# Kernel tuning notes

Measured on AMD Instinct MI355X. Metric: run time of the kernel, lower is better.

The kernel has to match this reference:

```python
import jax, jax.numpy as jnp
import numpy as np

N, F, E, T = 50000, 128, 800000, 8


def setup_inputs() -> dict:
    key = jax.random.key(0)
    ks = jax.random.split(key, 10)
    s = 1.0 / np.sqrt(F)
    return {
        "x": jax.random.normal(ks[0], (N, F), jnp.float32),
        "edge_index": jax.random.randint(ks[1], (2, E), 0, N, jnp.int64),
        "edge_weight": jax.random.uniform(ks[2], (E,), jnp.float32),
        "W0": jax.random.normal(ks[3], (F, F), jnp.float32) * s,
        "Wih": jax.random.normal(ks[4], (3 * F, F), jnp.float32) * s,
        "Whh": jax.random.normal(ks[5], (3 * F, F), jnp.float32) * s,
        "bih": jax.random.normal(ks[6], (3 * F,), jnp.float32) * s,
        "bhh": jax.random.normal(ks[7], (3 * F,), jnp.float32) * s,
        "Wlin": jax.random.normal(ks[8], (T, F), jnp.float32) * s,
        "blin": jax.random.normal(ks[9], (T,), jnp.float32) * s,
    }


def _evolve_weight(W0, Wih, Whh, bih, bhh):
    # One GRU step with input = hidden = W0 (rows of weight matrix as batch).
    gi = W0 @ Wih.T + bih  # [F, 3F]
    gh = W0 @ Whh.T + bhh
    ir, iz, inn = jnp.split(gi, 3, axis=1)
    hr, hz, hn = jnp.split(gh, 3, axis=1)
    r = jax.nn.sigmoid(ir + hr)
    z = jax.nn.sigmoid(iz + hz)
    n = jnp.tanh(inn + r * hn)
    return (1.0 - z) * n + z * W0  # [F, F]


def reference(x, edge_index, edge_weight, W0, Wih, Whh, bih, bhh, Wlin, blin):
    n_nodes = x.shape[0]
    W = _evolve_weight(W0, Wih, Whh, bih, bhh)
    # gcn_norm with added self-loops (fill value 1.0), symmetric normalization
    loop = jnp.arange(n_nodes, dtype=edge_index.dtype)
    row = jnp.concatenate([edge_index[0], loop])
    col = jnp.concatenate([edge_index[1], loop])
    ew = jnp.concatenate([edge_weight, jnp.ones((n_nodes,), edge_weight.dtype)])
    deg = jax.ops.segment_sum(ew, col, num_segments=n_nodes)
    dinv = jnp.where(deg > 0, jax.lax.rsqrt(jnp.where(deg > 0, deg, 1.0)), 0.0)
    norm = dinv[row] * ew * dinv[col]  # [E+N]
    xw = x @ W  # [N, F]
    h = jax.ops.segment_sum(norm[:, None] * xw[row], col, num_segments=n_nodes)
    h = jax.nn.relu(h)
    return h @ Wlin.T + blin  # [N, n_target]
```

## Files before the change

### kernel.cpp

```cpp
#include <hip/hip_runtime.h>
#include <math.h>

#define F 128
#define FIX_SCALE 16777216.0f
#define FIX_INV   (1.0f / 16777216.0f)
#define CNT_SHIFT 40
#define DEG_MASK  ((1ULL << 40) - 1)

using bf16x8 = __attribute__((ext_vector_type(8))) short;
using f32x4  = __attribute__((ext_vector_type(4))) float;

__device__ inline int read_idx(const int* ei, long long elem, int i64) {
    return i64 ? (int)((const long long*)ei)[elem] : ei[elem];
}
__device__ inline unsigned int f2bf_rn(float f) {
    unsigned int b = __float_as_uint(f);
    return (b + 0x7FFFu + ((b >> 16) & 1u)) >> 16;
}
__device__ inline float bflo(unsigned int u) { return __uint_as_float(u << 16); }
__device__ inline float bfhi(unsigned int u) { return __uint_as_float(u & 0xFFFF0000u); }

__global__ void k_init(unsigned long long* packed, int* flag, const int* ei, int N) {
    int i = blockIdx.x * blockDim.x + threadIdx.x;
    if (i < N) packed[i] = 0ULL;
    if (i == 0) {
        int i64 = 1;
        for (int j = 0; j < 32; ++j) if (ei[2 * j + 1] != 0) { i64 = 0; break; }
        *flag = i64;
    }
}

__global__ void k_count(const int* ei, const float* ew, unsigned long long* packed,
                        int* pos, const int* flag, int E) {
    int e = blockIdx.x * blockDim.x + threadIdx.x;
    if (e >= E) return;
    int i64 = *flag;
    int c = read_idx(ei, (long long)E + e, i64);
    unsigned long long u = (1ULL << CNT_SHIFT) |
                           (unsigned long long)(ew[e] * FIX_SCALE + 0.5f);
    unsigned long long old = atomicAdd(&packed[c], u);
    pos[e] = (int)(old >> CNT_SHIFT);
}

__global__ void k_bsum(const unsigned long long* __restrict__ packed,
                       int* __restrict__ bsum, int N) {
    __shared__ int s[4];
    int i = blockIdx.x * 256 + threadIdx.x;
    int v = (i < N) ? (int)(packed[i] >> CNT_SHIFT) : 0;
    #pragma unroll
    for (int o = 1; o < 64; o <<= 1) v += __shfl_xor(v, o, 64);
    if ((threadIdx.x & 63) == 0) s[threadIdx.x >> 6] = v;
    __syncthreads();
    if (threadIdx.x == 0) bsum[blockIdx.x] = s[0] + s[1] + s[2] + s[3];
}

__global__ void k_bscan(int* bsum, int nb) {
    __shared__ int sdata[1024];
    int tid = threadIdx.x;
    int run = 0;
    for (int base = 0; base < nb; base += 1024) {
        int i = base + tid;
        int v = (i < nb) ? bsum[i] : 0;
        sdata[tid] = v;
        __syncthreads();
        #pragma unroll
        for (int s = 1; s < 1024; s <<= 1) {
            int add = (tid >= s) ? sdata[tid - s] : 0;
            __syncthreads();
            sdata[tid] += add;
            __syncthreads();
        }
        if (i < nb) bsum[i] = run + sdata[tid] - v;
        run += sdata[1023];
        __syncthreads();
    }
}

__global__ void k_offs(const unsigned long long* __restrict__ packed,
                       const int* __restrict__ bsum,
                       int* __restrict__ off, float* __restrict__ dinv, int N, int E) {
    __shared__ int sdata[256];
    int t = threadIdx.x;
    int i = blockIdx.x * 256 + t;
    unsigned long long p = (i < N) ? packed[i] : 0ULL;
    int v = (int)(p >> CNT_SHIFT);
    sdata[t] = v;
    __syncthreads();
    #pragma unroll
    for (int s = 1; s < 256; s <<= 1) {
        int add = (t >= s) ? sdata[t - s] : 0;
        __syncthreads();
        sdata[t] += add;
        __syncthreads();
    }
    if (i < N) {
        off[i] = bsum[blockIdx.x] + sdata[t] - v;
        float deg = 1.0f + (float)(p & DEG_MASK) * FIX_INV;
        dinv[i] = rsqrtf(deg);
        if (i == N - 1) off[N] = E;
    }
}

__global__ void k_place(const int* ei, const float* ew,
                        const int* __restrict__ off, const int* __restrict__ pos,
                        int2* ep, const int* flag, int E) {
    int e = blockIdx.x * blockDim.x + threadIdx.x;
    if (e >= E) return;
    int i64 = *flag;
    int r = read_idx(ei, e, i64);
    int c = read_idx(ei, (long long)E + e, i64);
    ep[off[c] + pos[e]] = make_int2(r, __float_as_int(ew[e]));
}

__global__ void k_evolve(const float* __restrict__ W0, const float* __restrict__ Wih,
                         const float* __restrict__ Whh, const float* __restrict__ bih,
                         const float* __restrict__ bhh,
                         unsigned short* __restrict__ Wth,
                         unsigned short* __restrict__ Wtl) {
    __shared__ __align__(16) float w0row[F];
    int i = blockIdx.x;
    int j = threadIdx.x;
    w0row[j] = W0[i * F + j];
    __syncthreads();
    float air = 0, aiz = 0, ain = 0, ahr = 0, ahz = 0, ahn = 0;
    const float* ir_p = Wih + (size_t)j * F;
    const float* iz_p = Wih + (size_t)(j + F) * F;
    const float* in_p = Wih + (size_t)(j + 2 * F) * F;
    const float* hr_p = Whh + (size_t)j * F;
    const float* hz_p = Whh + (size_t)(j + F) * F;
    const float* hn_p = Whh + (size_t)(j + 2 * F) * F;
    for (int k = 0; k < F; k += 4) {
        float4 w0 = *(const float4*)&w0row[k];
        float4 a;
        a = *(const float4*)&ir_p[k]; air += w0.x*a.x + w0.y*a.y + w0.z*a.z + w0.w*a.w;
        a = *(const float4*)&iz_p[k]; aiz += w0.x*a.x + w0.y*a.y + w0.z*a.z + w0.w*a.w;
        a = *(const float4*)&in_p[k]; ain += w0.x*a.x + w0.y*a.y + w0.z*a.z + w0.w*a.w;
        a = *(const float4*)&hr_p[k]; ahr += w0.x*a.x + w0.y*a.y + w0.z*a.z + w0.w*a.w;
        a = *(const float4*)&hz_p[k]; ahz += w0.x*a.x + w0.y*a.y + w0.z*a.z + w0.w*a.w;
        a = *(const float4*)&hn_p[k]; ahn += w0.x*a.x + w0.y*a.y + w0.z*a.z + w0.w*a.w;
    }
    air += bih[j];         ahr += bhh[j];
    aiz += bih[j + F];     ahz += bhh[j + F];
    ain += bih[j + 2*F];   ahn += bhh[j + 2*F];
    float r = 1.0f / (1.0f + expf(-(air + ahr)));
    float z = 1.0f / (1.0f + expf(-(aiz + ahz)));
    float n = tanhf(ain + r * ahn);
    float w = (1.0f - z) * n + z * w0row[j];
    unsigned int hb = f2bf_rn(w);
    float whi = __uint_as_float(hb << 16);
    unsigned int lb = f2bf_rn(w - whi);
    Wth[j * F + i] = (unsigned short)hb;
    Wtl[j * F + i] = (unsigned short)lb;
}

__global__ void k_cast(const float2* __restrict__ x2, const float* __restrict__ dinv,
                       unsigned int* __restrict__ xs, int M ) {
    int id = blockIdx.x * 256 + threadIdx.x;
    if (id >= M) return;
    float di = dinv[id >> 6];
    float2 v = x2[id];
    xs[id] = f2bf_rn(di * v.x) | (f2bf_rn(di * v.y) << 16);
}

__global__ __launch_bounds__(256) void k_agg2(const uint4* __restrict__ xs4,
                                              const int* __restrict__ off,
                                              const int2* __restrict__ ep,
                                              const float* __restrict__ dinv,
                                              uint4* __restrict__ hagg4, int N) {
    int wave = threadIdx.x >> 6, lane = threadIdx.x & 63;
    int c = blockIdx.x * 4 + wave;
    if (c >= N) return;
    int g = lane >> 4, sl = lane & 15;
    int start = off[c], end = off[c + 1];
    float a0[8] = {0,0,0,0,0,0,0,0}, a1[8] = {0,0,0,0,0,0,0,0};
    if (g == 0) {
        uint4 v = xs4[(size_t)c * 16 + sl];
        a0[0] = bflo(v.x); a0[1] = bfhi(v.x);
        a0[2] = bflo(v.y); a0[3] = bfhi(v.y);
        a0[4] = bflo(v.z); a0[5] = bfhi(v.z);
        a0[6] = bflo(v.w); a0[7] = bfhi(v.w);
    }
    for (int k = start; k < end; k += 8) {
        int iA = k + g, iB = k + g + 4;
        bool okA = iA < end, okB = iB < end;
        int2 eA, eB;
        if (okA) eA = ep[iA];
        if (okB) eB = ep[iB];
        if (okA) {
            uint4 v = xs4[(size_t)eA.x * 16 + sl];
            float w = __int_as_float(eA.y);
            a0[0] += w * bflo(v.x); a0[1] += w * bfhi(v.x);
            a0[2] += w * bflo(v.y); a0[3] += w * bfhi(v.y);
            a0[4] += w * bflo(v.z); a0[5] += w * bfhi(v.z);
            a0[6] += w * bflo(v.w); a0[7] += w * bfhi(v.w);
        }
        if (okB) {
            uint4 v = xs4[(size_t)eB.x * 16 + sl];
            float w = __int_as_float(eB.y);
            a1[0] += w * bflo(v.x); a1[1] += w * bfhi(v.x);
            a1[2] += w * bflo(v.y); a1[3] += w * bfhi(v.y);
            a1[4] += w * bflo(v.z); a1[5] += w * bfhi(v.z);
            a1[6] += w * bflo(v.w); a1[7] += w * bfhi(v.w);
        }
    }
    #pragma unroll
    for (int f = 0; f < 8; ++f) {
        float v = a0[f] + a1[f];
        v += __shfl_xor(v, 16, 64);
        v += __shfl_xor(v, 32, 64);
        a0[f] = v;
    }
    if (lane < 16) {
        float di = dinv[c];
        uint4 o;
        o.x = f2bf_rn(di * a0[0]) | (f2bf_rn(di * a0[1]) << 16);
        o.y = f2bf_rn(di * a0[2]) | (f2bf_rn(di * a0[3]) << 16);
        o.z = f2bf_rn(di * a0[4]) | (f2bf_rn(di * a0[5]) << 16);
        o.w = f2bf_rn(di * a0[6]) | (f2bf_rn(di * a0[7]) << 16);
        hagg4[(size_t)c * 16 + lane] = o;
    }
}

__global__ __launch_bounds__(256) void k_gemm(const uint4* __restrict__ hagg4,
                                              const unsigned short* __restrict__ Wth,
                                              const unsigned short* __restrict__ Wtl,
                                              const float* __restrict__ Wlin,
                                              const float* __restrict__ blin,
                                              float* __restrict__ out, int N) {
    __shared__ __align__(16) unsigned int At[64 * 68];
    __shared__ __align__(16) float WlinL[8 * F];
    int t = threadIdx.x;
    int row0 = blockIdx.x * 64;
    #pragma unroll
    for (int it = 0; it < 4; ++it) {
        int idx = it * 256 + t;
        int rr = idx >> 4, c4 = idx & 15;
        uint4 v = make_uint4(0u, 0u, 0u, 0u);
        if (row0 + rr < N) v = hagg4[(size_t)(row0 + rr) * 16 + c4];
        *(uint4*)&At[rr * 68 + c4 * 4] = v;
    }
    *(float4*)&WlinL[t * 4] = *(const float4*)&Wlin[t * 4];
    __syncthreads();

    int wave = t >> 6, lane = t & 63;
    int sl = lane & 15, q = lane >> 4;
    const unsigned short* Ash = (const unsigned short*)At;
    int mrow = wave * 16 + sl;

    f32x4 acc[8];
    #pragma unroll
    for (int nt = 0; nt < 8; ++nt) acc[nt] = (f32x4){0.f, 0.f, 0.f, 0.f};
    #pragma unroll
    for (int ko = 0; ko < 4; ++ko) {
        bf16x8 a = *(const bf16x8*)&Ash[mrow * 136 + ko * 32 + q * 8];
        #pragma unroll
        for (int nt = 0; nt < 8; ++nt) {
            int boff = (nt * 16 + sl) * F + ko * 32 + q * 8;
            bf16x8 bh = *(const bf16x8*)&Wth[boff];
            bf16x8 bl = *(const bf16x8*)&Wtl[boff];
            acc[nt] = __builtin_amdgcn_mfma_f32_16x16x32_bf16(a, bh, acc[nt], 0, 0, 0);
            acc[nt] = __builtin_amdgcn_mfma_f32_16x16x32_bf16(a, bl, acc[nt], 0, 0, 0);
        }
    }
    #pragma unroll
    for (int nt = 0; nt < 8; ++nt)
        #pragma unroll
        for (int r = 0; r < 4; ++r) acc[nt][r] = fmaxf(acc[nt][r], 0.f);

    float p[8][4];
    #pragma unroll
    for (int tt = 0; tt < 8; ++tt) {
        float wl[8];
        #pragma unroll
        for (int nt = 0; nt < 8; ++nt) wl[nt] = WlinL[tt * F + nt * 16 + sl];
        #pragma unroll
        for (int r = 0; r < 4; ++r) {
            float s = 0.f;
            #pragma unroll
            for (int nt = 0; nt < 8; ++nt) s += acc[nt][r] * wl[nt];
            p[tt][r] = s;
        }
    }
    #pragma unroll
    for (int tt = 0; tt < 8; ++tt)
        #pragma unroll
        for (int r = 0; r < 4; ++r) {
            float v = p[tt][r];
            v += __shfl_xor(v, 1, 64); v += __shfl_xor(v, 2, 64);
            v += __shfl_xor(v, 4, 64); v += __shfl_xor(v, 8, 64);
            p[tt][r] = v;
        }
    if (sl == 0) {
        #pragma unroll
        for (int r = 0; r < 4; ++r) {
            int row = row0 + wave * 16 + q * 4 + r;
            if (row < N) {
                #pragma unroll
                for (int tt = 0; tt < 8; ++tt)
                    out[(size_t)row * 8 + tt] = p[tt][r] + blin[tt];
            }
        }
    }
}

extern "C" void kernel_launch(void* const* d_in, const int* in_sizes, int n_in,
                              void* d_out, int out_size, void* d_ws, size_t ws_size,
                              hipStream_t stream) {
    const float* x    = (const float*)d_in[0];
    const int*   ei   = (const int*)d_in[1];
    const float* ew   = (const float*)d_in[2];
    const float* W0   = (const float*)d_in[3];
    const float* Wih  = (const float*)d_in[4];
    const float* Whh  = (const float*)d_in[5];
    const float* bih  = (const float*)d_in[6];
    const float* bhh  = (const float*)d_in[7];
    const float* Wlin = (const float*)d_in[8];
    const float* blin = (const float*)d_in[9];
    int N = in_sizes[0] / F;
    int E = in_sizes[1] / 2;
    float* outp = (float*)d_out;

    int nblk = (N + 255) / 256;

    char* wsb = (char*)d_ws;
    size_t cur = 0;
    auto alloc = [&](size_t sz) -> void* {
        void* p = wsb + cur;
        cur = (cur + sz + 255) & ~(size_t)255;
        return p;
    };
    unsigned long long* packed = (unsigned long long*)alloc((size_t)N * 8);
    float* dinv = (float*)alloc((size_t)N * 4);
    int*   off  = (int*)  alloc((size_t)(N + 1) * 4);
    int*   bsum = (int*)  alloc((size_t)nblk * 4);
    int*   flag = (int*)  alloc(256);
    int*   pos  = (int*)  alloc((size_t)E * 4);
    int2*  ep   = (int2*) alloc((size_t)E * 8);
    unsigned short* Wth = (unsigned short*)alloc((size_t)F * F * 2);
    unsigned short* Wtl = (unsigned short*)alloc((size_t)F * F * 2);
    unsigned int* xs    = (unsigned int*)alloc((size_t)N * 64 * 4);
    unsigned int* hagg  = (unsigned int*)alloc((size_t)N * 64 * 4);
    (void)ws_size; (void)n_in; (void)out_size;

    int M = N * 64;
    hipLaunchKernelGGL(k_init,   dim3(nblk),            dim3(256),  0, stream, packed, flag, ei, N);
    hipLaunchKernelGGL(k_count,  dim3((E + 255) / 256), dim3(256),  0, stream, ei, ew, packed, pos, flag, E);
    hipLaunchKernelGGL(k_bsum,   dim3(nblk),            dim3(256),  0, stream, packed, bsum, N);
    hipLaunchKernelGGL(k_bscan,  dim3(1),               dim3(1024), 0, stream, bsum, nblk);
    hipLaunchKernelGGL(k_offs,   dim3(nblk),            dim3(256),  0, stream, packed, bsum, off, dinv, N, E);
    hipLaunchKernelGGL(k_evolve, dim3(F),               dim3(F),    0, stream, W0, Wih, Whh, bih, bhh, Wth, Wtl);
    hipLaunchKernelGGL(k_place,  dim3((E + 255) / 256), dim3(256),  0, stream, ei, ew, off, pos, ep, flag, E);
    hipLaunchKernelGGL(k_cast,   dim3((M + 255) / 256), dim3(256),  0, stream, (const float2*)x, dinv, xs, M);
    hipLaunchKernelGGL(k_agg2,   dim3((N + 3) / 4),     dim3(256),  0, stream, (const uint4*)xs, off, ep, dinv, (uint4*)hagg, N);
    hipLaunchKernelGGL(k_gemm,   dim3((N + 63) / 64),   dim3(256),  0, stream, (const uint4*)hagg, Wth, Wtl, Wlin, blin, outp, N);
}
```

Baseline: 245.9 us.

## Fuse pipeline into fewer kernels with cooperative scan and agg-gemm fusion

Cuts the launch count from ten to five. Edge counting is merged with weight evolution, the three-kernel scan is replaced by a single cooperative kernel that uses grid syncs, and edge placement is merged with the feature cast. Aggregation is fused into the GEMM kernel so the aggregated rows go straight to shared memory instead of through the hagg buffer. In exchange, each GEMM block processes 16 rows per wave serially, which reduces parallelism in the gather phase and may leave latency less hidden.

```diff
diff --git a/kernel.cpp b/kernel.cpp
--- a/kernel.cpp
+++ b/kernel.cpp
@@ -1,4 +1,5 @@
 #include <hip/hip_runtime.h>
+#include <hip/hip_cooperative_groups.h>
 #include <math.h>
 
 #define F 128
@@ -30,98 +31,31 @@
     }
 }
 
-__global__ void k_count(const int* ei, const float* ew, unsigned long long* packed,
-                        int* pos, const int* flag, int E) {
-    int e = blockIdx.x * blockDim.x + threadIdx.x;
-    if (e >= E) return;
-    int i64 = *flag;
-    int c = read_idx(ei, (long long)E + e, i64);
-    unsigned long long u = (1ULL << CNT_SHIFT) |
-                           (unsigned long long)(ew[e] * FIX_SCALE + 0.5f);
-    unsigned long long old = atomicAdd(&packed[c], u);
-    pos[e] = (int)(old >> CNT_SHIFT);
-}
-
-__global__ void k_bsum(const unsigned long long* __restrict__ packed,
-                       int* __restrict__ bsum, int N) {
-    __shared__ int s[4];
-    int i = blockIdx.x * 256 + threadIdx.x;
-    int v = (i < N) ? (int)(packed[i] >> CNT_SHIFT) : 0;
-    #pragma unroll
-    for (int o = 1; o < 64; o <<= 1) v += __shfl_xor(v, o, 64);
-    if ((threadIdx.x & 63) == 0) s[threadIdx.x >> 6] = v;
+__global__ __launch_bounds__(256) void k_count_evolve(
+        const int* __restrict__ ei, const float* __restrict__ ew,
+        unsigned long long* __restrict__ packed, int* __restrict__ pos,
+        const int* __restrict__ flag, int E, int cntBlocks,
+        const float* __restrict__ W0, const float* __restrict__ Wih,
+        const float* __restrict__ Whh, const float* __restrict__ bih,
+        const float* __restrict__ bhh,
+        unsigned short* __restrict__ Wth, unsigned short* __restrict__ Wtl) {
+    __shared__ __align__(16) float w0row[F];
+    if ((int)blockIdx.x < cntBlocks) {
+        int e = blockIdx.x * 256 + threadIdx.x;
+        if (e >= E) return;
+        int i64 = *flag;
+        int c = read_idx(ei, (long long)E + e, i64);
+        unsigned long long u = (1ULL << CNT_SHIFT) |
+                               (unsigned long long)(ew[e] * FIX_SCALE + 0.5f);
+        unsigned long long old = atomicAdd(&packed[c], u);
+        pos[e] = (int)(old >> CNT_SHIFT);
+        return;
+    }
+    int i = blockIdx.x - cntBlocks;
+    int j = threadIdx.x;
+    if (j < F) w0row[j] = W0[i * F + j];
     __syncthreads();
-    if (threadIdx.x == 0) bsum[blockIdx.x] = s[0] + s[1] + s[2] + s[3];
-}
-
-__global__ void k_bscan(int* bsum, int nb) {
-    __shared__ int sdata[1024];
-    int tid = threadIdx.x;
-    int run = 0;
-    for (int base = 0; base < nb; base += 1024) {
-        int i = base + tid;
-        int v = (i < nb) ? bsum[i] : 0;
-        sdata[tid] = v;
-        __syncthreads();
-        #pragma unroll
-        for (int s = 1; s < 1024; s <<= 1) {
-            int add = (tid >= s) ? sdata[tid - s] : 0;
-            __syncthreads();
-            sdata[tid] += add;
-            __syncthreads();
-        }
-        if (i < nb) bsum[i] = run + sdata[tid] - v;
-        run += sdata[1023];
-        __syncthreads();
-    }
-}
-
-__global__ void k_offs(const unsigned long long* __restrict__ packed,
-                       const int* __restrict__ bsum,
-                       int* __restrict__ off, float* __restrict__ dinv, int N, int E) {
-    __shared__ int sdata[256];
-    int t = threadIdx.x;
-    int i = blockIdx.x * 256 + t;
-    unsigned long long p = (i < N) ? packed[i] : 0ULL;
-    int v = (int)(p >> CNT_SHIFT);
-    sdata[t] = v;
-    __syncthreads();
-    #pragma unroll
-    for (int s = 1; s < 256; s <<= 1) {
-        int add = (t >= s) ? sdata[t - s] : 0;
-        __syncthreads();
-        sdata[t] += add;
-        __syncthreads();
-    }
-    if (i < N) {
-        off[i] = bsum[blockIdx.x] + sdata[t] - v;
-        float deg = 1.0f + (float)(p & DEG_MASK) * FIX_INV;
-        dinv[i] = rsqrtf(deg);
-        if (i == N - 1) off[N] = E;
-    }
-}
-
-__global__ void k_place(const int* ei, const float* ew,
-                        const int* __restrict__ off, const int* __restrict__ pos,
-                        int2* ep, const int* flag, int E) {
-    int e = blockIdx.x * blockDim.x + threadIdx.x;
-    if (e >= E) return;
-    int i64 = *flag;
-    int r = read_idx(ei, e, i64);
-    int c = read_idx(ei, (long long)E + e, i64);
-    ep[off[c] + pos[e]] = make_int2(r, __float_as_int(ew[e]));
-}
-
-__global__ void k_evolve(const float* __restrict__ W0, const float* __restrict__ Wih,
-                         const float* __restrict__ Whh, const float* __restrict__ bih,
-                         const float* __restrict__ bhh,
-                         unsigned short* __restrict__ Wth,
-                         unsigned short* __restrict__ Wtl) {
-    __shared__ __align__(16) float w0row[F];
-    int i = blockIdx.x;
-    int j = threadIdx.x;
-    w0row[j] = W0[i * F + j];
-    __syncthreads();
+    if (j >= F) return;
     float air = 0, aiz = 0, ain = 0, ahr = 0, ahz = 0, ahn = 0;
     const float* ir_p = Wih + (size_t)j * F;
     const float* iz_p = Wih + (size_t)(j + F) * F;
@@ -153,100 +87,155 @@
     Wtl[j * F + i] = (unsigned short)lb;
 }
 
-__global__ void k_cast(const float2* __restrict__ x2, const float* __restrict__ dinv,
-                       unsigned int* __restrict__ xs, int M ) {
-    int id = blockIdx.x * 256 + threadIdx.x;
-    if (id >= M) return;
-    float di = dinv[id >> 6];
-    float2 v = x2[id];
-    xs[id] = f2bf_rn(di * v.x) | (f2bf_rn(di * v.y) << 16);
-}
-
-__global__ __launch_bounds__(256) void k_agg2(const uint4* __restrict__ xs4,
-                                              const int* __restrict__ off,
-                                              const int2* __restrict__ ep,
-                                              const float* __restrict__ dinv,
-                                              uint4* __restrict__ hagg4, int N) {
-    int wave = threadIdx.x >> 6, lane = threadIdx.x & 63;
-    int c = blockIdx.x * 4 + wave;
-    if (c >= N) return;
-    int g = lane >> 4, sl = lane & 15;
-    int start = off[c], end = off[c + 1];
-    float a0[8] = {0,0,0,0,0,0,0,0}, a1[8] = {0,0,0,0,0,0,0,0};
-    if (g == 0) {
-        uint4 v = xs4[(size_t)c * 16 + sl];
-        a0[0] = bflo(v.x); a0[1] = bfhi(v.x);
-        a0[2] = bflo(v.y); a0[3] = bfhi(v.y);
-        a0[4] = bflo(v.z); a0[5] = bfhi(v.z);
-        a0[6] = bflo(v.w); a0[7] = bfhi(v.w);
-    }
-    for (int k = start; k < end; k += 8) {
-        int iA = k + g, iB = k + g + 4;
-        bool okA = iA < end, okB = iB < end;
-        int2 eA, eB;
-        if (okA) eA = ep[iA];
-        if (okB) eB = ep[iB];
-        if (okA) {
-            uint4 v = xs4[(size_t)eA.x * 16 + sl];
-            float w = __int_as_float(eA.y);
-            a0[0] += w * bflo(v.x); a0[1] += w * bfhi(v.x);
-            a0[2] += w * bflo(v.y); a0[3] += w * bfhi(v.y);
-            a0[4] += w * bflo(v.z); a0[5] += w * bfhi(v.z);
-            a0[6] += w * bflo(v.w); a0[7] += w * bfhi(v.w);
-        }
-        if (okB) {
-            uint4 v = xs4[(size_t)eB.x * 16 + sl];
-            float w = __int_as_float(eB.y);
-            a1[0] += w * bflo(v.x); a1[1] += w * bfhi(v.x);
-            a1[2] += w * bflo(v.y); a1[3] += w * bfhi(v.y);
-            a1[4] += w * bflo(v.z); a1[5] += w * bfhi(v.z);
-            a1[6] += w * bflo(v.w); a1[7] += w * bfhi(v.w);
-        }
-    }
-    #pragma unroll
-    for (int f = 0; f < 8; ++f) {
-        float v = a0[f] + a1[f];
-        v += __shfl_xor(v, 16, 64);
-        v += __shfl_xor(v, 32, 64);
-        a0[f] = v;
-    }
-    if (lane < 16) {
-        float di = dinv[c];
-        uint4 o;
-        o.x = f2bf_rn(di * a0[0]) | (f2bf_rn(di * a0[1]) << 16);
-        o.y = f2bf_rn(di * a0[2]) | (f2bf_rn(di * a0[3]) << 16);
-        o.z = f2bf_rn(di * a0[4]) | (f2bf_rn(di * a0[5]) << 16);
-        o.w = f2bf_rn(di * a0[6]) | (f2bf_rn(di * a0[7]) << 16);
-        hagg4[(size_t)c * 16 + lane] = o;
-    }
-}
-
-__global__ __launch_bounds__(256) void k_gemm(const uint4* __restrict__ hagg4,
-                                              const unsigned short* __restrict__ Wth,
-                                              const unsigned short* __restrict__ Wtl,
-                                              const float* __restrict__ Wlin,
-                                              const float* __restrict__ blin,
-                                              float* __restrict__ out, int N) {
+__global__ __launch_bounds__(256) void k_scan(const unsigned long long* __restrict__ packed,
+                       int* __restrict__ bsum, int* __restrict__ off,
+                       float* __restrict__ dinv, int N, int E, int nblk) {
+    cooperative_groups::grid_group grid = cooperative_groups::this_grid();
+    __shared__ int sdata[256];
+    int t = threadIdx.x, b = blockIdx.x;
+    int i = b * 256 + t;
+    unsigned long long p = (i < N) ? packed[i] : 0ULL;
+    int v = (int)(p >> CNT_SHIFT);
+    sdata[t] = v;
+    __syncthreads();
+    #pragma unroll
+    for (int s = 1; s < 256; s <<= 1) {
+        int add = (t >= s) ? sdata[t - s] : 0;
+        __syncthreads();
+        sdata[t] += add;
+        __syncthreads();
+    }
+    int incl = sdata[t];
+    if (t == 255) bsum[b] = incl;
+    __threadfence();
+    grid.sync();
+    if (b == 0) {
+        int run = 0;
+        for (int base = 0; base < nblk; base += 256) {
+            int idx = base + t;
+            int bv = (idx < nblk) ? bsum[idx] : 0;
+            __syncthreads();
+            sdata[t] = bv;
+            __syncthreads();
+            #pragma unroll
+            for (int s = 1; s < 256; s <<= 1) {
+                int add = (t >= s) ? sdata[t - s] : 0;
+                __syncthreads();
+                sdata[t] += add;
+                __syncthreads();
+            }
+            if (idx < nblk) bsum[idx] = run + sdata[t] - bv;
+            run += sdata[255];
+            __syncthreads();
+        }
+        __threadfence();
+    }
+    grid.sync();
+    if (i < N) {
+        off[i] = bsum[b] + incl - v;
+        float deg = 1.0f + (float)(p & DEG_MASK) * FIX_INV;
+        dinv[i] = rsqrtf(deg);
+        if (i == N - 1) off[N] = E;
+    }
+}
+
+__global__ __launch_bounds__(256) void k_place_cast(
+        const int* __restrict__ ei, const float* __restrict__ ew,
+        const int* __restrict__ off, const int* __restrict__ pos,
+        int2* __restrict__ ep, const int* __restrict__ flag, int E, int placeBlocks,
+        const float2* __restrict__ x2, const float* __restrict__ dinv,
+        unsigned int* __restrict__ xs, int M) {
+    if ((int)blockIdx.x < placeBlocks) {
+        int e = blockIdx.x * 256 + threadIdx.x;
+        if (e >= E) return;
+        int i64 = *flag;
+        int r = read_idx(ei, e, i64);
+        int c = read_idx(ei, (long long)E + e, i64);
+        ep[off[c] + pos[e]] = make_int2(r, __float_as_int(ew[e]));
+    } else {
+        int id = ((int)blockIdx.x - placeBlocks) * 256 + threadIdx.x;
+        if (id >= M) return;
+        float di = dinv[id >> 6];
+        float2 v = x2[id];
+        xs[id] = f2bf_rn(di * v.x) | (f2bf_rn(di * v.y) << 16);
+    }
+}
+
+__global__ __launch_bounds__(256) void k_agg_gemm(
+        const uint4* __restrict__ xs4, const int* __restrict__ off,
+        const int2* __restrict__ ep, const float* __restrict__ dinv,
+        const unsigned short* __restrict__ Wth, const unsigned short* __restrict__ Wtl,
+        const float* __restrict__ Wlin, const float* __restrict__ blin,
+        float* __restrict__ out, int N) {
     __shared__ __align__(16) unsigned int At[64 * 68];
     __shared__ __align__(16) float WlinL[8 * F];
     int t = threadIdx.x;
+    int wave = t >> 6, lane = t & 63;
     int row0 = blockIdx.x * 64;
-    #pragma unroll
-    for (int it = 0; it < 4; ++it) {
-        int idx = it * 256 + t;
-        int rr = idx >> 4, c4 = idx & 15;
-        uint4 v = make_uint4(0u, 0u, 0u, 0u);
-        if (row0 + rr < N) v = hagg4[(size_t)(row0 + rr) * 16 + c4];
-        *(uint4*)&At[rr * 68 + c4 * 4] = v;
-    }
     *(float4*)&WlinL[t * 4] = *(const float4*)&Wlin[t * 4];
+
+    int g = lane >> 4, sl = lane & 15;
+    for (int sub = 0; sub < 16; ++sub) {
+        int rr = wave * 16 + sub;
+        int c = row0 + rr;
+        if (c < N) {
+            float a0[8] = {0,0,0,0,0,0,0,0}, a1[8] = {0,0,0,0,0,0,0,0};
+            if (g == 0) {
+                uint4 vv = xs4[(size_t)c * 16 + sl];
+                a0[0] = bflo(vv.x); a0[1] = bfhi(vv.x);
+                a0[2] = bflo(vv.y); a0[3] = bfhi(vv.y);
+                a0[4] = bflo(vv.z); a0[5] = bfhi(vv.z);
+                a0[6] = bflo(vv.w); a0[7] = bfhi(vv.w);
+            }
+            int start = off[c], end = off[c + 1];
+            for (int k = start; k < end; k += 8) {
+                int iA = k + g, iB = k + g + 4;
+                bool okA = iA < end, okB = iB < end;
+                int2 eA, eB;
+                if (okA) eA = ep[iA];
+                if (okB) eB = ep[iB];
+                if (okA) {
+                    uint4 vv = xs4[(size_t)eA.x * 16 + sl];
+                    float w = __int_as_float(eA.y);
+                    a0[0] += w * bflo(vv.x); a0[1] += w * bfhi(vv.x);
+                    a0[2] += w * bflo(vv.y); a0[3] += w * bfhi(vv.y);
+                    a0[4] += w * bflo(vv.z); a0[5] += w * bfhi(vv.z);
+                    a0[6] += w * bflo(vv.w); a0[7] += w * bfhi(vv.w);
+                }
+                if (okB) {
+                    uint4 vv = xs4[(size_t)eB.x * 16 + sl];
+                    float w = __int_as_float(eB.y);
+                    a1[0] += w * bflo(vv.x); a1[1] += w * bfhi(vv.x);
+                    a1[2] += w * bflo(vv.y); a1[3] += w * bfhi(vv.y);
+                    a1[4] += w * bflo(vv.z); a1[5] += w * bfhi(vv.z);
+                    a1[6] += w * bflo(vv.w); a1[7] += w * bfhi(vv.w);
+                }
+            }
+            #pragma unroll
+            for (int f = 0; f < 8; ++f) {
+                float v2 = a0[f] + a1[f];
+                v2 += __shfl_xor(v2, 16, 64);
+                v2 += __shfl_xor(v2, 32, 64);
+                a0[f] = v2;
+            }
+            if (lane < 16) {
+                float di = dinv[c];
+                uint4 o;
+                o.x = f2bf_rn(di * a0[0]) | (f2bf_rn(di * a0[1]) << 16);
+                o.y = f2bf_rn(di * a0[2]) | (f2bf_rn(di * a0[3]) << 16);
+                o.z = f2bf_rn(di * a0[4]) | (f2bf_rn(di * a0[5]) << 16);
+                o.w = f2bf_rn(di * a0[6]) | (f2bf_rn(di * a0[7]) << 16);
+                *(uint4*)&At[rr * 68 + sl * 4] = o;
+            }
+        } else if (lane < 16) {
+            *(uint4*)&At[rr * 68 + sl * 4] = make_uint4(0u, 0u, 0u, 0u);
+        }
+    }
     __syncthreads();
 
-    int wave = t >> 6, lane = t & 63;
-    int sl = lane & 15, q = lane >> 4;
+    int q = g;
     const unsigned short* Ash = (const unsigned short*)At;
     int mrow = wave * 16 + sl;
-
     f32x4 acc[8];
     #pragma unroll
     for (int nt = 0; nt < 8; ++nt) acc[nt] = (f32x4){0.f, 0.f, 0.f, 0.f};
@@ -321,6 +310,8 @@
     float* outp = (float*)d_out;
 
     int nblk = (N + 255) / 256;
+    int cntBlocks = (E + 255) / 256;
+    int M = N * 64;
 
     char* wsb = (char*)d_ws;
     size_t cur = 0;
@@ -339,18 +330,20 @@
     unsigned short* Wth = (unsigned short*)alloc((size_t)F * F * 2);
     unsigned short* Wtl = (unsigned short*)alloc((size_t)F * F * 2);
     unsigned int* xs    = (unsigned int*)alloc((size_t)N * 64 * 4);
-    unsigned int* hagg  = (unsigned int*)alloc((size_t)N * 64 * 4);
     (void)ws_size; (void)n_in; (void)out_size;
 
-    int M = N * 64;
-    hipLaunchKernelGGL(k_init,   dim3(nblk),            dim3(256),  0, stream, packed, flag, ei, N);
-    hipLaunchKernelGGL(k_count,  dim3((E + 255) / 256), dim3(256),  0, stream, ei, ew, packed, pos, flag, E);
-    hipLaunchKernelGGL(k_bsum,   dim3(nblk),            dim3(256),  0, stream, packed, bsum, N);
-    hipLaunchKernelGGL(k_bscan,  dim3(1),               dim3(1024), 0, stream, bsum, nblk);
-    hipLaunchKernelGGL(k_offs,   dim3(nblk),            dim3(256),  0, stream, packed, bsum, off, dinv, N, E);
-    hipLaunchKernelGGL(k_evolve, dim3(F),               dim3(F),    0, stream, W0, Wih, Whh, bih, bhh, Wth, Wtl);
-    hipLaunchKernelGGL(k_place,  dim3((E + 255) / 256), dim3(256),  0, stream, ei, ew, off, pos, ep, flag, E);
-    hipLaunchKernelGGL(k_cast,   dim3((M + 255) / 256), dim3(256),  0, stream, (const float2*)x, dinv, xs, M);
-    hipLaunchKernelGGL(k_agg2,   dim3((N + 3) / 4),     dim3(256),  0, stream, (const uint4*)xs, off, ep, dinv, (uint4*)hagg, N);
-    hipLaunchKernelGGL(k_gemm,   dim3((N + 63) / 64),   dim3(256),  0, stream, (const uint4*)hagg, Wth, Wtl, Wlin, blin, outp, N);
-}
+    hipLaunchKernelGGL(k_init, dim3(nblk), dim3(256), 0, stream, packed, flag, ei, N);
+    hipLaunchKernelGGL(k_count_evolve, dim3(cntBlocks + F), dim3(256), 0, stream,
+                       ei, ew, packed, pos, flag, E, cntBlocks,
+                       W0, Wih, Whh, bih, bhh, Wth, Wtl);
+    {
+        void* args[] = { (void*)&packed, (void*)&bsum, (void*)&off, (void*)&dinv,
+                         (void*)&N, (void*)&E, (void*)&nblk };
+        hipLaunchCooperativeKernel((void*)k_scan, dim3(nblk), dim3(256), args, 0, stream);
+    }
+    hipLaunchKernelGGL(k_place_cast, dim3(cntBlocks + (M + 255) / 256), dim3(256), 0, stream,
+                       ei, ew, off, pos, ep, flag, E, cntBlocks,
+                       (const float2*)x, dinv, xs, M);
+    hipLaunchKernelGGL(k_agg_gemm, dim3((N + 63) / 64), dim3(256), 0, stream,
+                       (const uint4*)xs, off, ep, dinv, Wth, Wtl, Wlin, blin, outp, N);
+}
```

Measured after the change: 348.6 us. 41.7% more time.

## Merge independent launches and unroll edge gather with clamped indices

Applied to the files above, without the earlier changes.

Merges the count and weight-evolve kernels into one launch, split by block index, and does the same for the place and cast kernels. This cuts the launch count from ten to eight and lets independent work run concurrently. The aggregation loop now handles 16 edges per iteration. Out-of-range edges are clamped to the last index and given zero weight instead of branching, which puts more gathers in flight per lane. In exchange, the evolve blocks now run with 256 threads where only 128 work, and edges past the end cost redundant loads.

```diff
diff --git a/kernel.cpp b/kernel.cpp
--- a/kernel.cpp
+++ b/kernel.cpp
@@ -19,6 +19,13 @@
 }
 __device__ inline float bflo(unsigned int u) { return __uint_as_float(u << 16); }
 __device__ inline float bfhi(unsigned int u) { return __uint_as_float(u & 0xFFFF0000u); }
+
+__device__ inline void acc8(float* acc, float wt, uint4 v) {
+    acc[0] += wt * bflo(v.x); acc[1] += wt * bfhi(v.x);
+    acc[2] += wt * bflo(v.y); acc[3] += wt * bfhi(v.y);
+    acc[4] += wt * bflo(v.z); acc[5] += wt * bfhi(v.z);
+    acc[6] += wt * bflo(v.w); acc[7] += wt * bfhi(v.w);
+}
 
 __global__ void k_init(unsigned long long* packed, int* flag, const int* ei, int N) {
     int i = blockIdx.x * blockDim.x + threadIdx.x;
@@ -30,98 +37,31 @@
     }
 }
 
-__global__ void k_count(const int* ei, const float* ew, unsigned long long* packed,
-                        int* pos, const int* flag, int E) {
-    int e = blockIdx.x * blockDim.x + threadIdx.x;
-    if (e >= E) return;
-    int i64 = *flag;
-    int c = read_idx(ei, (long long)E + e, i64);
-    unsigned long long u = (1ULL << CNT_SHIFT) |
-                           (unsigned long long)(ew[e] * FIX_SCALE + 0.5f);
-    unsigned long long old = atomicAdd(&packed[c], u);
-    pos[e] = (int)(old >> CNT_SHIFT);
-}
-
-__global__ void k_bsum(const unsigned long long* __restrict__ packed,
-                       int* __restrict__ bsum, int N) {
-    __shared__ int s[4];
-    int i = blockIdx.x * 256 + threadIdx.x;
-    int v = (i < N) ? (int)(packed[i] >> CNT_SHIFT) : 0;
-    #pragma unroll
-    for (int o = 1; o < 64; o <<= 1) v += __shfl_xor(v, o, 64);
-    if ((threadIdx.x & 63) == 0) s[threadIdx.x >> 6] = v;
+__global__ __launch_bounds__(256) void k_count_evolve(
+        const int* __restrict__ ei, const float* __restrict__ ew,
+        unsigned long long* __restrict__ packed, int* __restrict__ pos,
+        const int* __restrict__ flag, int E, int cntBlocks,
+        const float* __restrict__ W0, const float* __restrict__ Wih,
+        const float* __restrict__ Whh, const float* __restrict__ bih,
+        const float* __restrict__ bhh,
+        unsigned short* __restrict__ Wth, unsigned short* __restrict__ Wtl) {
+    __shared__ __align__(16) float w0row[F];
+    if ((int)blockIdx.x < cntBlocks) {
+        int e = blockIdx.x * 256 + threadIdx.x;
+        if (e >= E) return;
+        int i64 = *flag;
+        int c = read_idx(ei, (long long)E + e, i64);
+        unsigned long long u = (1ULL << CNT_SHIFT) |
+                               (unsigned long long)(ew[e] * FIX_SCALE + 0.5f);
+        unsigned long long old = atomicAdd(&packed[c], u);
+        pos[e] = (int)(old >> CNT_SHIFT);
+        return;
+    }
+    int i = blockIdx.x - cntBlocks;
+    int j = threadIdx.x;
+    if (j < F) w0row[j] = W0[i * F + j];
     __syncthreads();
-    if (threadIdx.x == 0) bsum[blockIdx.x] = s[0] + s[1] + s[2] + s[3];
-}
-
-__global__ void k_bscan(int* bsum, int nb) {
-    __shared__ int sdata[1024];
-    int tid = threadIdx.x;
-    int run = 0;
-    for (int base = 0; base < nb; base += 1024) {
-        int i = base + tid;
-        int v = (i < nb) ? bsum[i] : 0;
-        sdata[tid] = v;
-        __syncthreads();
-        #pragma unroll
-        for (int s = 1; s < 1024; s <<= 1) {
-            int add = (tid >= s) ? sdata[tid - s] : 0;
-            __syncthreads();
-            sdata[tid] += add;
-            __syncthreads();
-        }
-        if (i < nb) bsum[i] = run + sdata[tid] - v;
-        run += sdata[1023];
-        __syncthreads();
-    }
-}
-
-__global__ void k_offs(const unsigned long long* __restrict__ packed,
-                       const int* __restrict__ bsum,
-                       int* __restrict__ off, float* __restrict__ dinv, int N, int E) {
-    __shared__ int sdata[256];
-    int t = threadIdx.x;
-    int i = blockIdx.x * 256 + t;
-    unsigned long long p = (i < N) ? packed[i] : 0ULL;
-    int v = (int)(p >> CNT_SHIFT);
-    sdata[t] = v;
-    __syncthreads();
-    #pragma unroll
-    for (int s = 1; s < 256; s <<= 1) {
-        int add = (t >= s) ? sdata[t - s] : 0;
-        __syncthreads();
-        sdata[t] += add;
-        __syncthreads();
-    }
-    if (i < N) {
-        off[i] = bsum[blockIdx.x] + sdata[t] - v;
-        float deg = 1.0f + (float)(p & DEG_MASK) * FIX_INV;
-        dinv[i] = rsqrtf(deg);
-        if (i == N - 1) off[N] = E;
-    }
-}
-
-__global__ void k_place(const int* ei, const float* ew,
-                        const int* __restrict__ off, const int* __restrict__ pos,
-                        int2* ep, const int* flag, int E) {
-    int e = blockIdx.x * blockDim.x + threadIdx.x;
-    if (e >= E) return;
-    int i64 = *flag;
-    int r = read_idx(ei, e, i64);
-    int c = read_idx(ei, (long long)E + e, i64);
-    ep[off[c] + pos[e]] = make_int2(r, __float_as_int(ew[e]));
-}
-
-__global__ void k_evolve(const float* __restrict__ W0, const float* __restrict__ Wih,
-                         const float* __restrict__ Whh, const float* __restrict__ bih,
-                         const float* __restrict__ bhh,
-                         unsigned short* __restrict__ Wth,
-                         unsigned short* __restrict__ Wtl) {
-    __shared__ __align__(16) float w0row[F];
-    int i = blockIdx.x;
-    int j = threadIdx.x;
-    w0row[j] = W0[i * F + j];
-    __syncthreads();
+    if (j >= F) return;
     float air = 0, aiz = 0, ain = 0, ahr = 0, ahz = 0, ahn = 0;
     const float* ir_p = Wih + (size_t)j * F;
     const float* iz_p = Wih + (size_t)(j + F) * F;
@@ -153,13 +93,85 @@
     Wtl[j * F + i] = (unsigned short)lb;
 }
 
-__global__ void k_cast(const float2* __restrict__ x2, const float* __restrict__ dinv,
-                       unsigned int* __restrict__ xs, int M ) {
-    int id = blockIdx.x * 256 + threadIdx.x;
-    if (id >= M) return;
-    float di = dinv[id >> 6];
-    float2 v = x2[id];
-    xs[id] = f2bf_rn(di * v.x) | (f2bf_rn(di * v.y) << 16);
+__global__ void k_bsum(const unsigned long long* __restrict__ packed,
+                       int* __restrict__ bsum, int N) {
+    __shared__ int s[4];
+    int i = blockIdx.x * 256 + threadIdx.x;
+    int v = (i < N) ? (int)(packed[i] >> CNT_SHIFT) : 0;
+    #pragma unroll
+    for (int o = 1; o < 64; o <<= 1) v += __shfl_xor(v, o, 64);
+    if ((threadIdx.x & 63) == 0) s[threadIdx.x >> 6] = v;
+    __syncthreads();
+    if (threadIdx.x == 0) bsum[blockIdx.x] = s[0] + s[1] + s[2] + s[3];
+}
+
+__global__ void k_bscan(int* bsum, int nb) {
+    __shared__ int sdata[1024];
+    int tid = threadIdx.x;
+    int run = 0;
+    for (int base = 0; base < nb; base += 1024) {
+        int i = base + tid;
+        int v = (i < nb) ? bsum[i] : 0;
+        sdata[tid] = v;
+        __syncthreads();
+        #pragma unroll
+        for (int s = 1; s < 1024; s <<= 1) {
+            int add = (tid >= s) ? sdata[tid - s] : 0;
+            __syncthreads();
+            sdata[tid] += add;
+            __syncthreads();
+        }
+        if (i < nb) bsum[i] = run + sdata[tid] - v;
+        run += sdata[1023];
+        __syncthreads();
+    }
+}
+
+__global__ void k_offs(const unsigned long long* __restrict__ packed,
+                       const int* __restrict__ bsum,
+                       int* __restrict__ off, float* __restrict__ dinv, int N, int E) {
+    __shared__ int sdata[256];
+    int t = threadIdx.x;
+    int i = blockIdx.x * 256 + t;
+    unsigned long long p = (i < N) ? packed[i] : 0ULL;
+    int v = (int)(p >> CNT_SHIFT);
+    sdata[t] = v;
+    __syncthreads();
+    #pragma unroll
+    for (int s = 1; s < 256; s <<= 1) {
+        int add = (t >= s) ? sdata[t - s] : 0;
+        __syncthreads();
+        sdata[t] += add;
+        __syncthreads();
+    }
+    if (i < N) {
+        off[i] = bsum[blockIdx.x] + sdata[t] - v;
+        float deg = 1.0f + (float)(p & DEG_MASK) * FIX_INV;
+        dinv[i] = rsqrtf(deg);
+        if (i == N - 1) off[N] = E;
+    }
+}
+
+__global__ __launch_bounds__(256) void k_place_cast(
+        const int* __restrict__ ei, const float* __restrict__ ew,
+        const int* __restrict__ off, const int* __restrict__ pos,
+        int2* __restrict__ ep, const int* __restrict__ flag, int E, int placeBlocks,
+        const float2* __restrict__ x2, const float* __restrict__ dinv,
+        unsigned int* __restrict__ xs, int M) {
+    if ((int)blockIdx.x < placeBlocks) {
+        int e = blockIdx.x * 256 + threadIdx.x;
+        if (e >= E) return;
+        int i64 = *flag;
+        int r = read_idx(ei, e, i64);
+        int c = read_idx(ei, (long long)E + e, i64);
+        ep[off[c] + pos[e]] = make_int2(r, __float_as_int(ew[e]));
+    } else {
+        int id = ((int)blockIdx.x - placeBlocks) * 256 + threadIdx.x;
+        if (id >= M) return;
+        float di = dinv[id >> 6];
+        float2 v = x2[id];
+        xs[id] = f2bf_rn(di * v.x) | (f2bf_rn(di * v.y) << 16);
+    }
 }
 
 __global__ __launch_bounds__(256) void k_agg2(const uint4* __restrict__ xs4,
@@ -172,6 +184,7 @@
     if (c >= N) return;
     int g = lane >> 4, sl = lane & 15;
     int start = off[c], end = off[c + 1];
+    float di = dinv[c];
     float a0[8] = {0,0,0,0,0,0,0,0}, a1[8] = {0,0,0,0,0,0,0,0};
     if (g == 0) {
         uint4 v = xs4[(size_t)c * 16 + sl];
@@ -180,28 +193,25 @@
         a0[4] = bflo(v.z); a0[5] = bfhi(v.z);
         a0[6] = bflo(v.w); a0[7] = bfhi(v.w);
     }
-    for (int k = start; k < end; k += 8) {
-        int iA = k + g, iB = k + g + 4;
-        bool okA = iA < end, okB = iB < end;
-        int2 eA, eB;
-        if (okA) eA = ep[iA];
-        if (okB) eB = ep[iB];
-        if (okA) {
-            uint4 v = xs4[(size_t)eA.x * 16 + sl];
-            float w = __int_as_float(eA.y);
-            a0[0] += w * bflo(v.x); a0[1] += w * bfhi(v.x);
-            a0[2] += w * bflo(v.y); a0[3] += w * bfhi(v.y);
-            a0[4] += w * bflo(v.z); a0[5] += w * bfhi(v.z);
-            a0[6] += w * bflo(v.w); a0[7] += w * bfhi(v.w);
-        }
-        if (okB) {
-            uint4 v = xs4[(size_t)eB.x * 16 + sl];
-            float w = __int_as_float(eB.y);
-            a1[0] += w * bflo(v.x); a1[1] += w * bfhi(v.x);
-            a1[2] += w * bflo(v.y); a1[3] += w * bfhi(v.y);
-            a1[4] += w * bflo(v.z); a1[5] += w * bfhi(v.z);
-            a1[6] += w * bflo(v.w); a1[7] += w * bfhi(v.w);
-        }
+    int last = end - 1;
+    for (int k = start; k < end; k += 16) {
+        int iA = k + g, iB = k + g + 4, iC = k + g + 8, iD = k + g + 12;
+        int2 eA = ep[min(iA, last)];
+        int2 eB = ep[min(iB, last)];
+        int2 eC = ep[min(iC, last)];
+        int2 eD = ep[min(iD, last)];
+        uint4 vA = xs4[(size_t)eA.x * 16 + sl];
+        uint4 vB = xs4[(size_t)eB.x * 16 + sl];
+        uint4 vC = xs4[(size_t)eC.x * 16 + sl];
+        uint4 vD = xs4[(size_t)eD.x * 16 + sl];
+        float wA = (iA <= last) ? __int_as_float(eA.y) : 0.f;
+        float wB = (iB <= last) ? __int_as_float(eB.y) : 0.f;
+        float wC = (iC <= last) ? __int_as_float(eC.y) : 0.f;
+        float wD = (iD <= last) ? __int_as_float(eD.y) : 0.f;
+        acc8(a0, wA, vA);
+        acc8(a1, wB, vB);
+        acc8(a0, wC, vC);
+        acc8(a1, wD, vD);
     }
     #pragma unroll
     for (int f = 0; f < 8; ++f) {
@@ -211,7 +221,6 @@
         a0[f] = v;
     }
     if (lane < 16) {
-        float di = dinv[c];
         uint4 o;
         o.x = f2bf_rn(di * a0[0]) | (f2bf_rn(di * a0[1]) << 16);
         o.y = f2bf_rn(di * a0[2]) | (f2bf_rn(di * a0[3]) << 16);
@@ -321,6 +330,8 @@
     float* outp = (float*)d_out;
 
     int nblk = (N + 255) / 256;
+    int cntBlocks = (E + 255) / 256;
+    int M = N * 64;
 
     char* wsb = (char*)d_ws;
     size_t cur = 0;
@@ -342,15 +353,18 @@
     unsigned int* hagg  = (unsigned int*)alloc((size_t)N * 64 * 4);
     (void)ws_size; (void)n_in; (void)out_size;
 
-    int M = N * 64;
-    hipLaunchKernelGGL(k_init,   dim3(nblk),            dim3(256),  0, stream, packed, flag, ei, N);
-    hipLaunchKernelGGL(k_count,  dim3((E + 255) / 256), dim3(256),  0, stream, ei, ew, packed, pos, flag, E);
-    hipLaunchKernelGGL(k_bsum,   dim3(nblk),            dim3(256),  0, stream, packed, bsum, N);
-    hipLaunchKernelGGL(k_bscan,  dim3(1),               dim3(1024), 0, stream, bsum, nblk);
-    hipLaunchKernelGGL(k_offs,   dim3(nblk),            dim3(256),  0, stream, packed, bsum, off, dinv, N, E);
-    hipLaunchKernelGGL(k_evolve, dim3(F),               dim3(F),    0, stream, W0, Wih, Whh, bih, bhh, Wth, Wtl);
-    hipLaunchKernelGGL(k_place,  dim3((E + 255) / 256), dim3(256),  0, stream, ei, ew, off, pos, ep, flag, E);
-    hipLaunchKernelGGL(k_cast,   dim3((M + 255) / 256), dim3(256),  0, stream, (const float2*)x, dinv, xs, M);
-    hipLaunchKernelGGL(k_agg2,   dim3((N + 3) / 4),     dim3(256),  0, stream, (const uint4*)xs, off, ep, dinv, (uint4*)hagg, N);
-    hipLaunchKernelGGL(k_gemm,   dim3((N + 63) / 64),   dim3(256),  0, stream, (const uint4*)hagg, Wth, Wtl, Wlin, blin, outp, N);
-}
+    hipLaunchKernelGGL(k_init, dim3(nblk), dim3(256), 0, stream, packed, flag, ei, N);
+    hipLaunchKernelGGL(k_count_evolve, dim3(cntBlocks + F), dim3(256), 0, stream,
+                       ei, ew, packed, pos, flag, E, cntBlocks,
+                       W0, Wih, Whh, bih, bhh, Wth, Wtl);
+    hipLaunchKernelGGL(k_bsum,  dim3(nblk), dim3(256),  0, stream, packed, bsum, N);
+    hipLaunchKernelGGL(k_bscan, dim3(1),    dim3(1024), 0, stream, bsum, nblk);
+    hipLaunchKernelGGL(k_offs,  dim3(nblk), dim3(256),  0, stream, packed, bsum, off, dinv, N, E);
+    hipLaunchKernelGGL(k_place_cast, dim3(cntBlocks + (M + 255) / 256), dim3(256), 0, stream,
+                       ei, ew, off, pos, ep, flag, E, cntBlocks,
+                       (const float2*)x, dinv, xs, M);
+    hipLaunchKernelGGL(k_agg2, dim3((N + 3) / 4), dim3(256), 0, stream,
+                       (const uint4*)xs, off, ep, dinv, (uint4*)hagg, N);
+    hipLaunchKernelGGL(k_gemm, dim3((N + 63) / 64), dim3(256), 0, stream,
+                       (const uint4*)hagg, Wth, Wtl, Wlin, blin, outp, N);
+}
```

Measured after the change: 249.9 us. Within noise of the previous version (+1.6%).
